# Optimization experiments

Hardware: AMD Instinct MI355X
Metric: run time of the kernel (lower is better)

## Reference

```python
import jax, jax.numpy as jnp
import numpy as np

B, N = 8, 256
DN, DE, H, Z, L = 16, 8, 64, 64, 3
FC = 128  # internal MLP width from the torch code


def _glorot(key, fan_in, fan_out, shape=None):
    if shape is None:
        shape = (fan_in, fan_out)
    r = np.sqrt(6.0 / (fan_in + fan_out)).astype(np.float32)
    return jax.random.uniform(key, shape, jnp.float32, -r, r)


def setup_inputs() -> dict:
    key = jax.random.key(0)
    ks = jax.random.split(key, 24)
    inp = {
        "adj": jax.random.uniform(ks[0], (B, N, N), jnp.float32),
        "node_feat": jax.random.normal(ks[1], (B, N, DN), jnp.float32),
        "edge_feat": jax.random.normal(ks[2], (B, N, N, DE), jnp.float32),
        "noise": jax.random.normal(ks[3], (B, N, Z), jnp.float32),
        # node / edge embedding MLPs
        "node_fc1_w": _glorot(ks[4], DN, FC), "node_fc1_b": jnp.zeros((FC,), jnp.float32),
        "node_fc2_w": _glorot(ks[5], FC, H), "node_fc2_b": jnp.zeros((H,), jnp.float32),
        "edge_fc1_w": _glorot(ks[6], DE, FC), "edge_fc1_b": jnp.zeros((FC,), jnp.float32),
        "edge_fc2_w": _glorot(ks[7], FC, H), "edge_fc2_b": jnp.zeros((H,), jnp.float32),
        # per-layer GCN weights (GraphConvSparse has no bias) and combine linears
        "gcn_w": _glorot(ks[8], H, H, (L, H, H)),
        "comb_w": _glorot(ks[9], 2 * H, H, (L, 2 * H, H)),
        "comb_b": jnp.zeros((L, H), jnp.float32),
        # mean / logvar heads over concatenated (L+1)*H features
        "mean_fc1_w": _glorot(ks[10], (L + 1) * H, FC), "mean_fc1_b": jnp.zeros((FC,), jnp.float32),
        "mean_fc2_w": _glorot(ks[11], FC, Z), "mean_fc2_b": jnp.zeros((Z,), jnp.float32),
        "logvar_fc1_w": _glorot(ks[12], (L + 1) * H, FC), "logvar_fc1_b": jnp.zeros((FC,), jnp.float32),
        "logvar_fc2_w": _glorot(ks[13], FC, Z), "logvar_fc2_b": jnp.zeros((Z,), jnp.float32),
    }
    return inp


def reference(adj, node_feat, edge_feat, noise,
              node_fc1_w, node_fc1_b, node_fc2_w, node_fc2_b,
              edge_fc1_w, edge_fc1_b, edge_fc2_w, edge_fc2_b,
              gcn_w, comb_w, comb_b,
              mean_fc1_w, mean_fc1_b, mean_fc2_w, mean_fc2_b,
              logvar_fc1_w, logvar_fc1_b, logvar_fc2_w, logvar_fc2_b):
    # node embedding: two fused linear+tanh
    nh = jnp.tanh(node_feat @ node_fc1_w + node_fc1_b)
    nh = jnp.tanh(nh @ node_fc2_w + node_fc2_b)            # [B,N,H]
    # edge embedding over rank-4 edge features
    eh = jnp.tanh(edge_feat @ edge_fc1_w + edge_fc1_b)
    eh = jnp.tanh(eh @ edge_fc2_w + edge_fc2_b)            # [B,N,N,H]

    all_hidden = [nh]
    hidden = nh
    for layer in range(L):  # small fixed layer count
        # GraphConvSparse: tanh(adj @ (x @ W))
        h = jnp.tanh(jnp.einsum('bij,bjh->bih', adj, hidden @ gcn_w[layer]))
        # edge-feature combine: contract over neighbor j and edge channel c
        comb = jnp.tanh(jnp.einsum('bijc,bjk->bik', eh, h))
        hidden = jnp.tanh(jnp.concatenate([h, comb], axis=2) @ comb_w[layer] + comb_b[layer])
        all_hidden.append(hidden)

    hcat = jnp.concatenate(all_hidden, axis=2)             # [B,N,(L+1)*H]
    mean = jnp.tanh(hcat @ mean_fc1_w + mean_fc1_b) @ mean_fc2_w + mean_fc2_b
    logvar = jnp.tanh(hcat @ logvar_fc1_w + logvar_fc1_b) @ logvar_fc2_w + logvar_fc2_b
    latent = noise * jnp.exp(0.5 * logvar) + mean
    return (latent, mean, logvar)
```

## Files before the change

### kernel.cpp

```cpp
#include <hip/hip_runtime.h>
#include <hip/hip_bf16.h>

#define B_    8
#define N_    256
#define DN_   16
#define DE_   8
#define H_    64
#define Z_    64
#define L_    3
#define FC_   128
#define ROWS_ (B_ * N_)
#define EDGES_ (B_ * N_ * N_)

__device__ __forceinline__ float fast_tanh(float x) {
    float e = __expf(2.0f * x);
    return 1.0f - 2.0f * __builtin_amdgcn_rcpf(e + 1.0f);
}

__global__ __launch_bounds__(128) void node_embed_kernel(
    const float* __restrict__ nf, const float* __restrict__ w1,
    const float* __restrict__ b1, const float* __restrict__ w2,
    const float* __restrict__ b2, float* __restrict__ hcat)
{
    int row = blockIdx.x;
    int t = threadIdx.x;
    __shared__ float x[DN_];
    __shared__ float hid[FC_];
    if (t < DN_) x[t] = nf[row * DN_ + t];
    __syncthreads();
    float a = b1[t];
#pragma unroll
    for (int c = 0; c < DN_; ++c) a += x[c] * w1[c * FC_ + t];
    hid[t] = fast_tanh(a);
    __syncthreads();
    if (t < H_) {
        float a2 = b2[t];
#pragma unroll
        for (int k = 0; k < FC_; ++k) a2 += hid[k] * w2[k * H_ + t];
        hcat[(size_t)row * 256 + t] = fast_tanh(a2);
    }
}

__global__ __launch_bounds__(256) void edge_mlp_kernel(
    const float* __restrict__ ef, const float* __restrict__ w1,
    const float* __restrict__ b1, const float* __restrict__ w2,
    const float* __restrict__ b2, float* __restrict__ ehs)
{
    int e = blockIdx.x * 256 + threadIdx.x;
    const float4* ep = (const float4*)(ef + (size_t)e * DE_);
    float4 x0 = ep[0], x1 = ep[1];
    float x[8] = {x0.x, x0.y, x0.z, x0.w, x1.x, x1.y, x1.z, x1.w};
    float acc[H_];
#pragma unroll
    for (int o = 0; o < H_; ++o) acc[o] = b2[o];
    for (int k = 0; k < FC_; ++k) {
        float hk = b1[k];
#pragma unroll
        for (int c = 0; c < DE_; ++c) hk += x[c] * w1[c * FC_ + k];
        hk = fast_tanh(hk);
        const float* w2r = w2 + k * H_;
#pragma unroll
        for (int o = 0; o < H_; ++o) acc[o] += hk * w2r[o];
    }
    float s = 0.f;
#pragma unroll
    for (int o = 0; o < H_; ++o) s += fast_tanh(acc[o]);
    ehs[e] = s;
}

__global__ __launch_bounds__(256) void gcn_kernel(
    const float* __restrict__ adj, const float* __restrict__ hcat,
    const float* __restrict__ gw, float* __restrict__ h, int seg)
{
    int wid = threadIdx.x >> 6;
    int lane = threadIdx.x & 63;
    int row = __builtin_amdgcn_readfirstlane(blockIdx.x * 4 + wid);
    int b = row >> 8;
    const float* arow = adj + (size_t)row * N_;
    const float* hb = hcat + (size_t)b * N_ * 256 + seg * H_;
    float g = 0.f;
    for (int j = 0; j < N_; ++j) g += arow[j] * hb[j * 256 + lane];
    __shared__ float gs[4][H_];
    gs[wid][lane] = g;
    __syncthreads();
    float a = 0.f;
#pragma unroll
    for (int k = 0; k < H_; ++k) a += gs[wid][k] * gw[k * H_ + lane];
    h[(size_t)row * H_ + lane] = fast_tanh(a);
}

__global__ __launch_bounds__(256) void comb_kernel(
    const float* __restrict__ ehs, const float* __restrict__ h,
    const float* __restrict__ cw, const float* __restrict__ cb,
    float* __restrict__ hcat, int seg)
{
    int wid = threadIdx.x >> 6;
    int lane = threadIdx.x & 63;
    int row = __builtin_amdgcn_readfirstlane(blockIdx.x * 4 + wid);
    int b = row >> 8;
    const float* er = ehs + (size_t)row * N_;
    const float* hb = h + (size_t)b * N_ * H_;
    float c = 0.f;
    for (int j = 0; j < N_; ++j) c += er[j] * hb[j * H_ + lane];
    c = fast_tanh(c);
    __shared__ float ch[4][H_], hi[4][H_];
    ch[wid][lane] = c;
    hi[wid][lane] = h[(size_t)row * H_ + lane];
    __syncthreads();
    float a = cb[lane];
#pragma unroll
    for (int k = 0; k < H_; ++k) a += hi[wid][k] * cw[k * H_ + lane];
#pragma unroll
    for (int k = 0; k < H_; ++k) a += ch[wid][k] * cw[(H_ + k) * H_ + lane];
    hcat[(size_t)row * 256 + (seg + 1) * H_ + lane] = fast_tanh(a);
}

__global__ __launch_bounds__(128) void head_kernel(
    const float* __restrict__ hcat, const float* __restrict__ noise,
    const float* __restrict__ m1w, const float* __restrict__ m1b,
    const float* __restrict__ m2w, const float* __restrict__ m2b,
    const float* __restrict__ v1w, const float* __restrict__ v1b,
    const float* __restrict__ v2w, const float* __restrict__ v2b,
    float* __restrict__ out)
{
    const int G = 8;
    int row0 = blockIdx.x * G;
    int t = threadIdx.x;
    __shared__ float rbT[256][G];
    __shared__ float hid[G][FC_];
    __shared__ float ms[G][H_];
    for (int idx = t; idx < 256 * G; idx += 128) {
        int k = idx >> 3, g = idx & 7;
        rbT[k][g] = hcat[(size_t)(row0 + g) * 256 + k];
    }
    __syncthreads();

    float acc[G];
#pragma unroll
    for (int g = 0; g < G; ++g) acc[g] = m1b[t];
    for (int k = 0; k < 256; ++k) {
        float w = m1w[k * FC_ + t];
        const float4* rp = (const float4*)&rbT[k][0];
        float4 r0 = rp[0], r1 = rp[1];
        acc[0] += r0.x * w; acc[1] += r0.y * w; acc[2] += r0.z * w; acc[3] += r0.w * w;
        acc[4] += r1.x * w; acc[5] += r1.y * w; acc[6] += r1.z * w; acc[7] += r1.w * w;
    }
#pragma unroll
    for (int g = 0; g < G; ++g) hid[g][t] = fast_tanh(acc[g]);
    __syncthreads();
    if (t < H_) {
#pragma unroll
        for (int g = 0; g < G; ++g) {
            float m = m2b[t];
            for (int k = 0; k < FC_; ++k) m += hid[g][k] * m2w[k * H_ + t];
            ms[g][t] = m;
            out[(size_t)ROWS_ * Z_ + (size_t)(row0 + g) * H_ + t] = m;
        }
    }
    __syncthreads();

#pragma unroll
    for (int g = 0; g < G; ++g) acc[g] = v1b[t];
    for (int k = 0; k < 256; ++k) {
        float w = v1w[k * FC_ + t];
        const float4* rp = (const float4*)&rbT[k][0];
        float4 r0 = rp[0], r1 = rp[1];
        acc[0] += r0.x * w; acc[1] += r0.y * w; acc[2] += r0.z * w; acc[3] += r0.w * w;
        acc[4] += r1.x * w; acc[5] += r1.y * w; acc[6] += r1.z * w; acc[7] += r1.w * w;
    }
#pragma unroll
    for (int g = 0; g < G; ++g) hid[g][t] = fast_tanh(acc[g]);
    __syncthreads();
    if (t < H_) {
#pragma unroll
        for (int g = 0; g < G; ++g) {
            float lv = v2b[t];
            for (int k = 0; k < FC_; ++k) lv += hid[g][k] * v2w[k * H_ + t];
            out[(size_t)2 * ROWS_ * Z_ + (size_t)(row0 + g) * H_ + t] = lv;
            float lat = noise[(size_t)(row0 + g) * H_ + t] * __expf(0.5f * lv) + ms[g][t];
            out[(size_t)(row0 + g) * H_ + t] = lat;
        }
    }
}

extern "C" void kernel_launch(void* const* d_in, const int* in_sizes, int n_in,
                              void* d_out, int out_size, void* d_ws, size_t ws_size,
                              hipStream_t stream)
{
    const float* adj   = (const float*)d_in[0];
    const float* nf    = (const float*)d_in[1];
    const float* ef    = (const float*)d_in[2];
    const float* noise = (const float*)d_in[3];
    const float* nw1 = (const float*)d_in[4];  const float* nb1 = (const float*)d_in[5];
    const float* nw2 = (const float*)d_in[6];  const float* nb2 = (const float*)d_in[7];
    const float* ew1 = (const float*)d_in[8];  const float* eb1 = (const float*)d_in[9];
    const float* ew2 = (const float*)d_in[10]; const float* eb2 = (const float*)d_in[11];
    const float* gw  = (const float*)d_in[12];
    const float* cw  = (const float*)d_in[13]; const float* cb = (const float*)d_in[14];
    const float* m1w = (const float*)d_in[15]; const float* m1b = (const float*)d_in[16];
    const float* m2w = (const float*)d_in[17]; const float* m2b = (const float*)d_in[18];
    const float* v1w = (const float*)d_in[19]; const float* v1b = (const float*)d_in[20];
    const float* v2w = (const float*)d_in[21]; const float* v2b = (const float*)d_in[22];

    float* out  = (float*)d_out;
    float* ws   = (float*)d_ws;
    float* hcat = ws;
    float* ehs  = ws + 524288;
    float* h    = ws + 1048576;

    hipLaunchKernelGGL(node_embed_kernel, dim3(ROWS_), dim3(128), 0, stream,
                       nf, nw1, nb1, nw2, nb2, hcat);
    hipLaunchKernelGGL(edge_mlp_kernel, dim3(EDGES_ / 256), dim3(256), 0, stream,
                       ef, ew1, eb1, ew2, eb2, ehs);
    for (int l = 0; l < L_; ++l) {
        hipLaunchKernelGGL(gcn_kernel, dim3(ROWS_ / 4), dim3(256), 0, stream,
                           adj, hcat, gw + l * H_ * H_, h, l);
        hipLaunchKernelGGL(comb_kernel, dim3(ROWS_ / 4), dim3(256), 0, stream,
                           ehs, h, cw + l * 2 * H_ * H_, cb + l * H_, hcat, l);
    }
    hipLaunchKernelGGL(head_kernel, dim3(ROWS_ / 8), dim3(128), 0, stream,
                       hcat, noise, m1w, m1b, m2w, m2b, v1w, v1b, v2w, v2b, out);
}
```

Baseline: 333.8 us.

## Run edge MLP second layer on bf16 MFMA with split-precision emulation

Replaces the per-thread scalar FP32 edge MLP with a block-level version. Each block first computes the 128-wide tanh hidden layer into LDS as hi/lo bf16 pairs using an XOR-swizzled layout, then runs the 128x64 second layer with 16x16x32 bf16 MFMA instructions. Three MFMAs per tile (hh, lh, hl) approximate FP32 accuracy. This targets the ALU-bound 8192-FMA-per-edge inner loop, which dominates runtime. It adds LDS use of 64KB per block and re-converts w2 to bf16 pairs in every block, and the hi/lo split keeps the error close to FP32 but not equal to it.

```diff
diff --git a/kernel.cpp b/kernel.cpp
--- a/kernel.cpp
+++ b/kernel.cpp
@@ -12,9 +12,21 @@
 #define ROWS_ (B_ * N_)
 #define EDGES_ (B_ * N_ * N_)
 
+using short8 = __attribute__((ext_vector_type(8))) short;
+using f32x4t = __attribute__((ext_vector_type(4))) float;
+
 __device__ __forceinline__ float fast_tanh(float x) {
     float e = __expf(2.0f * x);
     return 1.0f - 2.0f * __builtin_amdgcn_rcpf(e + 1.0f);
+}
+
+__device__ __forceinline__ unsigned short f2bf(float x) {
+    unsigned int u = __float_as_uint(x);
+    unsigned int r = (u + 0x7fffu + ((u >> 16) & 1u)) >> 16;
+    return (unsigned short)r;
+}
+__device__ __forceinline__ float bf2f(unsigned short u) {
+    return __uint_as_float(((unsigned int)u) << 16);
 }
 
 __global__ __launch_bounds__(128) void node_embed_kernel(
@@ -41,31 +53,105 @@
     }
 }
 
-__global__ __launch_bounds__(256) void edge_mlp_kernel(
+__global__ __launch_bounds__(128) void edge_mlp_mfma_kernel(
     const float* __restrict__ ef, const float* __restrict__ w1,
     const float* __restrict__ b1, const float* __restrict__ w2,
     const float* __restrict__ b2, float* __restrict__ ehs)
 {
-    int e = blockIdx.x * 256 + threadIdx.x;
-    const float4* ep = (const float4*)(ef + (size_t)e * DE_);
+    __shared__ unsigned short hh[128 * FC_];
+    __shared__ unsigned short hl[128 * FC_];
+
+    int t = threadIdx.x;
+    int lane = t & 63;
+    int wid = t >> 6;
+    size_t eb = (size_t)blockIdx.x * 128;
+    int el = t;
+    size_t e = eb + el;
+
+    const float4* ep = (const float4*)(ef + e * DE_);
     float4 x0 = ep[0], x1 = ep[1];
     float x[8] = {x0.x, x0.y, x0.z, x0.w, x1.x, x1.y, x1.z, x1.w};
-    float acc[H_];
-#pragma unroll
-    for (int o = 0; o < H_; ++o) acc[o] = b2[o];
-    for (int k = 0; k < FC_; ++k) {
-        float hk = b1[k];
-#pragma unroll
-        for (int c = 0; c < DE_; ++c) hk += x[c] * w1[c * FC_ + k];
-        hk = fast_tanh(hk);
-        const float* w2r = w2 + k * H_;
-#pragma unroll
-        for (int o = 0; o < H_; ++o) acc[o] += hk * w2r[o];
-    }
-    float s = 0.f;
-#pragma unroll
-    for (int o = 0; o < H_; ++o) s += fast_tanh(acc[o]);
-    ehs[e] = s;
+
+    for (int g = 0; g < 16; ++g) {
+        short8 ph, pl;
+#pragma unroll
+        for (int kb = 0; kb < 8; ++kb) {
+            int k = g * 8 + kb;
+            float a = b1[k];
+#pragma unroll
+            for (int c = 0; c < 8; ++c) a += x[c] * w1[c * FC_ + k];
+            float h = fast_tanh(a);
+            unsigned short hi = f2bf(h);
+            unsigned short lo = f2bf(h - bf2f(hi));
+            ph[kb] = (short)hi;
+            pl[kb] = (short)lo;
+        }
+        int slot = g ^ (el & 7);
+        *(short8*)&hh[el * FC_ + slot * 8] = ph;
+        *(short8*)&hl[el * FC_ + slot * 8] = pl;
+    }
+    __syncthreads();
+
+    int krow = (lane >> 4) * 8;
+    int col0 = lane & 15;
+    float b2v[4];
+#pragma unroll
+    for (int ot = 0; ot < 4; ++ot) b2v[ot] = b2[ot * 16 + col0];
+    f32x4t acc[4][4];
+#pragma unroll
+    for (int et = 0; et < 4; ++et)
+#pragma unroll
+        for (int ot = 0; ot < 4; ++ot)
+            acc[et][ot] = (f32x4t){b2v[et * 0 + ot] * 0.f + b2v[ot], b2v[ot], b2v[ot], b2v[ot]};
+
+#pragma unroll
+    for (int kk = 0; kk < 4; ++kk) {
+        short8 wh[4], wl[4];
+#pragma unroll
+        for (int ot = 0; ot < 4; ++ot) {
+#pragma unroll
+            for (int b = 0; b < 8; ++b) {
+                float v = w2[(kk * 32 + krow + b) * H_ + ot * 16 + col0];
+                unsigned short hi = f2bf(v);
+                unsigned short lo = f2bf(v - bf2f(hi));
+                wh[ot][b] = (short)hi;
+                wl[ot][b] = (short)lo;
+            }
+        }
+        short8 afh[4], afl[4];
+#pragma unroll
+        for (int et = 0; et < 4; ++et) {
+            int er = wid * 64 + et * 16 + (lane & 15);
+            int slot = (kk * 4 + (lane >> 4)) ^ (er & 7);
+            afh[et] = *(const short8*)&hh[er * FC_ + slot * 8];
+            afl[et] = *(const short8*)&hl[er * FC_ + slot * 8];
+        }
+#pragma unroll
+        for (int et = 0; et < 4; ++et)
+#pragma unroll
+            for (int ot = 0; ot < 4; ++ot) {
+                acc[et][ot] = __builtin_amdgcn_mfma_f32_16x16x32_bf16(
+                    afh[et], wh[ot], acc[et][ot], 0, 0, 0);
+                acc[et][ot] = __builtin_amdgcn_mfma_f32_16x16x32_bf16(
+                    afl[et], wh[ot], acc[et][ot], 0, 0, 0);
+                acc[et][ot] = __builtin_amdgcn_mfma_f32_16x16x32_bf16(
+                    afh[et], wl[ot], acc[et][ot], 0, 0, 0);
+            }
+    }
+
+#pragma unroll
+    for (int et = 0; et < 4; ++et)
+#pragma unroll
+        for (int r = 0; r < 4; ++r) {
+            float v = fast_tanh(acc[et][0][r]) + fast_tanh(acc[et][1][r])
+                    + fast_tanh(acc[et][2][r]) + fast_tanh(acc[et][3][r]);
+            v += __shfl_xor(v, 1);
+            v += __shfl_xor(v, 2);
+            v += __shfl_xor(v, 4);
+            v += __shfl_xor(v, 8);
+            if ((lane & 15) == 0)
+                ehs[eb + wid * 64 + et * 16 + (lane >> 4) * 4 + r] = v;
+        }
 }
 
 __global__ __launch_bounds__(256) void gcn_kernel(
@@ -210,7 +296,7 @@
 
     hipLaunchKernelGGL(node_embed_kernel, dim3(ROWS_), dim3(128), 0, stream,
                        nf, nw1, nb1, nw2, nb2, hcat);
-    hipLaunchKernelGGL(edge_mlp_kernel, dim3(EDGES_ / 256), dim3(256), 0, stream,
+    hipLaunchKernelGGL(edge_mlp_mfma_kernel, dim3(EDGES_ / 128), dim3(128), 0, stream,
                        ef, ew1, eb1, ew2, eb2, ehs);
     for (int l = 0; l < L_; ++l) {
         hipLaunchKernelGGL(gcn_kernel, dim3(ROWS_ / 4), dim3(256), 0, stream,
```

After: 360.8 us. 8.1% more time.
